# Performance work log

Measured on AMD Instinct MI355X. Metric: run time of the kernel, lower is better.

Reference implementation:

```python
import jax, jax.numpy as jnp
import numpy as np

B, S, E, D, H, L = 128, 50, 512, 1024, 16, 4
V, NU, NF, NR = 100000, 50000, 10000, 5
DK = D // H
FF = 4 * D


def _pe(S, D):
    # FranchisePositionalEncoding: two interleaved sin/cos halves (chrono + release*1.5)
    half = D // 2
    pos = jnp.arange(S, dtype=jnp.float32)[:, None]
    div = jnp.exp(jnp.arange(0, half, 2, dtype=jnp.float32) * (-np.log(10000.0) / half))
    def il(a):
        return jnp.stack([jnp.sin(a), jnp.cos(a)], axis=-1).reshape(S, half)
    return jnp.concatenate([il(pos * div), il(pos * div * 1.5)], axis=-1)  # [S, D]


def _ln(x, g, b):
    m = x.mean(-1, keepdims=True)
    v = ((x - m) ** 2).mean(-1, keepdims=True)
    return (x - m) * jax.lax.rsqrt(v + 1e-5) * g + b


def _gelu(x):
    return jax.nn.gelu(x, approximate=False)


def setup_inputs() -> dict:
    key = jax.random.key(0)
    ks = iter(jax.random.split(key, 64))
    def p(shape, s=0.02):
        return jax.random.normal(next(ks), shape, jnp.float32) * s
    inp = {
        'movie_table': p((V, E)), 'fran_table': p((NF, E)), 'entry_table': p((NR, E)),
        'proj_w': p((3 * E, D)), 'proj_b': jnp.zeros((D,), jnp.float32),
        'wq': p((L, D, D)), 'bq': jnp.zeros((L, D), jnp.float32),
        'wk': p((L, D, D)), 'bk': jnp.zeros((L, D), jnp.float32),
        'wv': p((L, D, D)), 'bv': jnp.zeros((L, D), jnp.float32),
        'wo': p((L, D, D)), 'bo': jnp.zeros((L, D), jnp.float32),
        'rel_table': p((L, NR, DK)),
        'aln_g': jnp.ones((L, D), jnp.float32), 'aln_b': jnp.zeros((L, D), jnp.float32),
        'f_w1': p((L, D, FF)), 'f_b1': jnp.zeros((L, FF), jnp.float32),
        'f_w2': p((L, FF, D)), 'f_b2': jnp.zeros((L, D), jnp.float32),
        'ln_g': jnp.ones((L, D), jnp.float32), 'ln_b': jnp.zeros((L, D), jnp.float32),
        'user_table': p((NU, D)),
        'mq_w': p((D, D)), 'mq_b': jnp.zeros((D,), jnp.float32),
        'mk_w': p((D, D)), 'mk_b': jnp.zeros((D,), jnp.float32),
        'mv_w': p((D, D)), 'mv_b': jnp.zeros((D,), jnp.float32),
        'mo_w': p((D, D)), 'mo_b': jnp.zeros((D,), jnp.float32),
        'c_w1': p((2 * D, D)), 'c_b1': jnp.zeros((D,), jnp.float32),
        'c_w2': p((D, 1)), 'c_b2': jnp.zeros((1,), jnp.float32),
        'n_w1': p((2 * D, D)), 'n_b1': jnp.zeros((D,), jnp.float32),
        'n_w2': p((D, V)), 'n_b2': jnp.zeros((V,), jnp.float32),
        'r_w1': p((3 * D, D)), 'r_b1': jnp.zeros((D,), jnp.float32),
        'r_w2': p((D, 1)), 'r_b2': jnp.zeros((1,), jnp.float32),
        'o_w1': p((D, D // 2)), 'o_b1': jnp.zeros((D // 2,), jnp.float32),
        'o_w2': p((D // 2, 2)), 'o_b2': jnp.zeros((2,), jnp.float32),
        'user_ids': jax.random.randint(next(ks), (B,), 0, NU),
        'movie_ids': jax.random.randint(next(ks), (B, S), 0, V),
        'franchise_ids': jax.random.randint(next(ks), (B, S), 0, NF),
        'entry_types': jax.random.randint(next(ks), (B, S), 0, NR),
        'relation_matrix': jax.random.randint(next(ks), (S, S), 0, NR),
    }
    return inp


def reference(movie_table, fran_table, entry_table, proj_w, proj_b,
              wq, bq, wk, bk, wv, bv, wo, bo, rel_table, aln_g, aln_b,
              f_w1, f_b1, f_w2, f_b2, ln_g, ln_b, user_table,
              mq_w, mq_b, mk_w, mk_b, mv_w, mv_b, mo_w, mo_b,
              c_w1, c_b1, c_w2, c_b2, n_w1, n_b1, n_w2, n_b2,
              r_w1, r_b1, r_w2, r_b2, o_w1, o_b1, o_w2, o_b2,
              user_ids, movie_ids, franchise_ids, entry_types, relation_matrix):
    b, s = movie_ids.shape
    d = proj_w.shape[1]
    nl, _, dk = rel_table.shape
    h = d // dk
    scale = 1.0 / np.sqrt(dk).astype(np.float32)

    # encoder input: concat(movie, franchise, entry) embeddings -> proj -> +PE
    x = jnp.concatenate([movie_table[movie_ids], fran_table[franchise_ids],
                         entry_table[entry_types]], axis=-1) @ proj_w + proj_b
    x = x + _pe(s, d)

    for l in range(nl):
        res = x
        q = (x @ wq[l] + bq[l]).reshape(b, s, h, dk).transpose(0, 2, 1, 3)  # [b,h,s,dk]
        k = (x @ wk[l] + bk[l]).reshape(b, s, h, dk).transpose(0, 2, 1, 3)
        v = (x @ wv[l] + bv[l]).reshape(b, s, h, dk).transpose(0, 2, 1, 3)
        scores = jnp.einsum('bhid,bhjd->bhij', q, k) * scale
        rel = rel_table[l][relation_matrix]  # [s,s,dk]
        scores = scores + 0.5 * jnp.einsum('bhid,ijd->bhij', q, rel)
        attn = jax.nn.softmax(scores, axis=-1)
        ctx = jnp.einsum('bhij,bhjd->bhid', attn, v).transpose(0, 2, 1, 3).reshape(b, s, d)
        x = _ln(ctx @ wo[l] + bo[l] + res, aln_g[l], aln_b[l])
        ff = _gelu(x @ f_w1[l] + f_b1[l]) @ f_w2[l] + f_b2[l]
        x = _ln(x + ff, ln_g[l], ln_b[l])

    # user preference cross-attention (nn.MultiheadAttention, q_len=1)
    user_emb = user_table[user_ids]  # [b,d]
    qh = (user_emb @ mq_w + mq_b).reshape(b, h, dk)
    kh = (x @ mk_w + mk_b).reshape(b, s, h, dk)
    vh = (x @ mv_w + mv_b).reshape(b, s, h, dk)
    a = jax.nn.softmax(jnp.einsum('bhd,bshd->bhs', qh, kh) * scale, axis=-1)
    user_pref = jnp.einsum('bhs,bshd->bhd', a, vh).reshape(b, d) @ mo_w + mo_b

    seq_repr = x.mean(axis=1)  # mask is None path
    ci = jnp.concatenate([user_pref, seq_repr], axis=-1)
    completion = jax.nn.sigmoid(_gelu(ci @ c_w1 + c_b1) @ c_w2 + c_b2)
    next_logits = _gelu(ci @ n_w1 + n_b1) @ n_w2 + n_b2
    ri = jnp.concatenate([user_emb, user_pref, seq_repr], axis=-1)
    rating = _gelu(ri @ r_w1 + r_b1) @ r_w2 + r_b2
    order = jax.nn.softmax(_gelu(user_pref @ o_w1 + o_b1) @ o_w2 + o_b2, axis=-1)
    return (x, completion, next_logits, rating, order, user_pref)
```

## Files before the change

### kernel.cpp

```cpp
#include <hip/hip_runtime.h>
#include <hip/hip_bf16.h>
#include <math.h>

#define B_   128
#define S_   50
#define BS_  (B_*S_)
#define E_   512
#define D_   1024
#define H_   16
#define DK_  64
#define L_   4
#define FF_  4096
#define V_   100000

typedef short bf8_t __attribute__((ext_vector_type(8)));
typedef float f32x4 __attribute__((ext_vector_type(4)));
typedef unsigned short u16;

__device__ __forceinline__ float gelu_exact(float x) {
    return 0.5f * x * (1.0f + erff(x * 0.70710678118654752440f));
}
__device__ __forceinline__ u16 f2bf(float f) {
    unsigned int u = __float_as_uint(f);
    return (u16)((u + 0x7FFFu + ((u >> 16) & 1u)) >> 16);
}
__device__ __forceinline__ float bf2f(u16 u) {
    return __uint_as_float(((unsigned int)u) << 16);
}

__device__ __forceinline__ void gload16(const u16* g, u16* l) {
    auto* g1 = reinterpret_cast<const __attribute__((address_space(1))) unsigned int*>(
                   reinterpret_cast<uintptr_t>(g));
    auto* l3 = reinterpret_cast<__attribute__((address_space(3))) unsigned int*>(
                   reinterpret_cast<uintptr_t>(l));
    __builtin_amdgcn_global_load_lds(g1, l3, 16, 0, 0);
}

__device__ __forceinline__ void wtrans_body(
    const float* __restrict__ W, u16* __restrict__ Wt,
    int K, int N, int nb, int kb, int dstRowOff)
{
    __shared__ float t[32][33];
    int c = threadIdx.x & 31, r0 = threadIdx.x >> 5;
    #pragma unroll
    for (int rr = 0; rr < 32; rr += 8)
        t[rr + r0][c] = W[(size_t)(kb + rr + r0) * N + nb + c];
    __syncthreads();
    #pragma unroll
    for (int rr = 0; rr < 32; rr += 8)
        Wt[(size_t)(dstRowOff + nb + rr + r0) * K + kb + c] = f2bf(t[c][rr + r0]);
}

__global__ __launch_bounds__(256) void wtrans(
    const float* __restrict__ W, u16* __restrict__ Wt,
    int K, int N, long srcLS, long dstLS, int dstRowOff)
{
    int l = blockIdx.z;
    wtrans_body(W + (size_t)l * srcLS, Wt + (size_t)l * dstLS,
                K, N, blockIdx.x * 32, blockIdx.y * 32, dstRowOff);
}

__global__ __launch_bounds__(256) void wtrans_qkv(
    const float* __restrict__ wq, const float* __restrict__ wk, const float* __restrict__ wv,
    u16* __restrict__ dst)
{
    int z = blockIdx.z;
    int l = z & 3, which = z >> 2;
    const float* W = (which == 0 ? wq : which == 1 ? wk : wv) + (size_t)l * (D_ * D_);
    u16* Wt = dst + (size_t)l * (3 * D_ * D_) + (size_t)which * (D_ * D_);
    wtrans_body(W, Wt, D_, D_, blockIdx.x * 32, blockIdx.y * 32, 0);
}

struct WT4 { const float* s[4]; u16* d[4]; };
__global__ __launch_bounds__(256) void wtrans4(WT4 p)
{
    int z = blockIdx.z;
    wtrans_body(p.s[z], p.d[z], D_, D_, blockIdx.x * 32, blockIdx.y * 32, 0);
}

__global__ __launch_bounds__(256) void wtrans_ff(
    const float* __restrict__ w1, const float* __restrict__ w2,
    u16* __restrict__ d1, u16* __restrict__ d2)
{
    if (blockIdx.z == 0)
        wtrans_body(w1, d1, D_, FF_, blockIdx.x * 32, blockIdx.y * 32, 0);
    else
        wtrans_body(w2, d2, FF_, D_, blockIdx.y * 32, blockIdx.x * 32, 0);
}

__global__ __launch_bounds__(256) void embed_concat(
    const float* __restrict__ mt, const float* __restrict__ ft, const float* __restrict__ et,
    const int* __restrict__ mids, const int* __restrict__ fids, const int* __restrict__ eids,
    u16* __restrict__ xinb)
{
    int bs = blockIdx.x;
    int mid = mids[bs], fid = fids[bs], eid = eids[bs];
    const float* srcs[3] = { mt + (size_t)mid * E_, ft + (size_t)fid * E_, et + (size_t)eid * E_ };
    u16* dst = xinb + (size_t)bs * (3 * E_);
    for (int i = threadIdx.x; i < 384; i += 256) {
        int seg = i >> 7, off = i & 127;
        float4 v = reinterpret_cast<const float4*>(srcs[seg])[off];
        ushort4 b;
        b.x = f2bf(v.x); b.y = f2bf(v.y); b.z = f2bf(v.z); b.w = f2bf(v.w);
        reinterpret_cast<ushort4*>(dst + seg * E_)[off] = b;
    }
}

__global__ __launch_bounds__(256) void pe_table(float* __restrict__ pet)
{
    int s = blockIdx.x;
    const float c = -logf(10000.0f) / 512.0f;
    for (int d = threadIdx.x; d < D_; d += 256) {
        int second = d >= 512;
        int cc = second ? d - 512 : d;
        int i = cc >> 1;
        float div = expf(c * (float)(2 * i));
        float a = (float)s * div * (second ? 1.5f : 1.0f);
        pet[s * D_ + d] = (cc & 1) ? cosf(a) : sinf(a);
    }
}

__global__ __launch_bounds__(256) void gemm_bf16(
    const u16* __restrict__ A, int lda, const u16* __restrict__ Wt,
    const float* __restrict__ bias, float* __restrict__ Cf,
    u16* __restrict__ Cb, int ldcb, u16* __restrict__ Cb2, int ldcb2,
    int M, int N, int K, int act, const float* __restrict__ pe)
{
    __shared__ u16 As[2 * 4096];
    __shared__ u16 Bs[2 * 4096];
    const int tid  = threadIdx.x;
    const int lane = tid & 63;
    const int wid  = tid >> 6;
    const int wr   = wid >> 1, wc = wid & 1;

    const int gx  = gridDim.x;
    const int nwg = gx * gridDim.y;
    {
    }
    int orig = blockIdx.y * gx + blockIdx.x;
    int qq = nwg >> 3, rr = nwg & 7, xcd = orig & 7, idx = orig >> 3;
    int wgid = (xcd < rr) ? (xcd * (qq + 1) + idx)
                          : (rr * (qq + 1) + (xcd - rr) * qq + idx);
    const int rowBase = (wgid / gx) * 128;
    const int colBase = (wgid % gx) * 128;

    const int fr = lane & 15;
    const int hi = lane >> 4;

    const int sRowL  = lane >> 2;
    const int sChunk = lane & 3;
    const int gRow0  = (wid << 5) + sRowL;
    const int skey   = (gRow0 >> 1) & 3;
    const int gC     = (sChunk ^ skey) << 3;
    const u16* aS0 = A  + (size_t)(rowBase + gRow0) * lda + gC;
    const u16* aS1 = aS0 + (size_t)16 * lda;
    const u16* bS0 = Wt + (size_t)(colBase + gRow0) * K + gC;
    const u16* bS1 = bS0 + (size_t)16 * K;
    const int ldsW0 = (wid << 5) << 5;
    const int ldsW1 = ldsW0 + (16 << 5);

    const int swz = ((hi ^ ((fr >> 1) & 3)) << 3);
    const int aRd = (wr * 64 + fr) * 32 + swz;
    const int bRd = (wc * 64 + fr) * 32 + swz;

    f32x4 acc[4][4] = {};
    const int nk = K >> 5;

    gload16(aS0, As + ldsW0);
    gload16(aS1, As + ldsW1);
    gload16(bS0, Bs + ldsW0);
    gload16(bS1, Bs + ldsW1);
    __builtin_amdgcn_sched_barrier(0);
    gload16(aS0 + 32, As + 4096 + ldsW0);
    gload16(aS1 + 32, As + 4096 + ldsW1);
    gload16(bS0 + 32, Bs + 4096 + ldsW0);
    gload16(bS1 + 32, Bs + 4096 + ldsW1);
    __builtin_amdgcn_sched_barrier(0);
    asm volatile("s_waitcnt vmcnt(4)\n\ts_barrier" ::: "memory");
    __builtin_amdgcn_sched_barrier(0);

    for (int t = 0; t < nk; ++t) {
        const int cur = t & 1;
        const u16* bA = As + cur * 4096;
        const u16* bB = Bs + cur * 4096;
        bf8_t af[4], bf[4];
        #pragma unroll
        for (int m = 0; m < 4; ++m)
            af[m] = *reinterpret_cast<const bf8_t*>(&bA[aRd + m * 512]);
        #pragma unroll
        for (int n = 0; n < 4; ++n)
            bf[n] = *reinterpret_cast<const bf8_t*>(&bB[bRd + n * 512]);
        #pragma unroll
        for (int m = 0; m < 4; ++m)
            #pragma unroll
            for (int n = 0; n < 4; ++n)
                acc[m][n] = __builtin_amdgcn_mfma_f32_16x16x32_bf16(af[m], bf[n], acc[m][n], 0, 0, 0);
        if (t == nk - 1) break;
        __builtin_amdgcn_sched_barrier(0);
        asm volatile("s_waitcnt lgkmcnt(0)\n\ts_barrier" ::: "memory");
        __builtin_amdgcn_sched_barrier(0);
        if (t + 2 < nk) {
            const int kb = (t + 2) << 5;
            u16* dA = As + cur * 4096;
            u16* dB = Bs + cur * 4096;
            gload16(aS0 + kb, dA + ldsW0);
            gload16(aS1 + kb, dA + ldsW1);
            gload16(bS0 + kb, dB + ldsW0);
            gload16(bS1 + kb, dB + ldsW1);
            __builtin_amdgcn_sched_barrier(0);
            asm volatile("s_waitcnt vmcnt(4)\n\ts_barrier" ::: "memory");
        } else {
            asm volatile("s_waitcnt vmcnt(0)\n\ts_barrier" ::: "memory");
        }
        __builtin_amdgcn_sched_barrier(0);
    }

    const int orow = (lane >> 4) << 2;
    #pragma unroll
    for (int m = 0; m < 4; ++m) {
        int r0 = rowBase + wr * 64 + m * 16 + orow;
        #pragma unroll
        for (int n = 0; n < 4; ++n) {
            int c = colBase + wc * 64 + n * 16 + fr;
            float bv = bias ? bias[c] : 0.0f;
            #pragma unroll
            for (int r = 0; r < 4; ++r) {
                float v = acc[m][n][r] + bv;
                if (act == 1) v = gelu_exact(v);
                if (pe) v += pe[(size_t)((r0 + r) % S_) * N + c];
                if (Cf)  Cf [(size_t)(r0 + r) * N + c] = v;
                if (Cb)  Cb [(size_t)(r0 + r) * ldcb  + c] = f2bf(v);
                if (Cb2) Cb2[(size_t)(r0 + r) * ldcb2 + c] = f2bf(v);
            }
        }
    }
}

__global__ __launch_bounds__(256) void gemm_logits(
    const float* __restrict__ A, int lda, const float* __restrict__ W,
    const float* __restrict__ bias, float* __restrict__ C, int N, int K)
{
    __shared__ u16 As[2][128][40];
    __shared__ u16 Bs[2][128][40];
    const int tid  = threadIdx.x;
    const int lane = tid & 63;
    const int wid  = tid >> 6;
    const int wr   = wid >> 1, wc = wid & 1;
    const int colBase = blockIdx.x * 128;

    const int a_r = tid >> 1;
    const int a_h = (tid & 1) << 4;
    const int b_c = tid & 127;
    const int b_h = (tid >> 7) << 4;

    const int fr = lane & 15;
    const int fk = (lane >> 4) << 3;

    f32x4 acc[4][4] = {};
    const int nvalid = N - colBase;
    const bool valid = b_c < nvalid;
    const int nk = K >> 5;

    float4 aR[4];
    float  bR[16];

    auto LD = [&](int kb) {
        const float* Ap = A + (size_t)a_r * lda + kb + a_h;
        #pragma unroll
        for (int q = 0; q < 4; ++q)
            aR[q] = *reinterpret_cast<const float4*>(Ap + q * 4);
        const float* Wp = W + (size_t)(kb + b_h) * N + colBase + b_c;
        #pragma unroll
        for (int kk = 0; kk < 16; ++kk)
            bR[kk] = valid ? Wp[(size_t)kk * N] : 0.0f;
    };
    auto ST = [&](int buf) {
        #pragma unroll
        for (int q = 0; q < 4; ++q) {
            ushort4 bb;
            bb.x = f2bf(aR[q].x); bb.y = f2bf(aR[q].y);
            bb.z = f2bf(aR[q].z); bb.w = f2bf(aR[q].w);
            *reinterpret_cast<ushort4*>(&As[buf][a_r][a_h + q * 4]) = bb;
        }
        u16 tmp[16];
        #pragma unroll
        for (int kk = 0; kk < 16; ++kk) tmp[kk] = f2bf(bR[kk]);
        *reinterpret_cast<bf8_t*>(&Bs[buf][b_c][b_h])     = *reinterpret_cast<const bf8_t*>(tmp);
        *reinterpret_cast<bf8_t*>(&Bs[buf][b_c][b_h + 8]) = *reinterpret_cast<const bf8_t*>(tmp + 8);
    };

    LD(0); ST(0);
    __syncthreads();

    for (int t = 0; t < nk; ++t) {
        if (t + 1 < nk) LD((t + 1) << 5);
        const int cur = t & 1;
        bf8_t af[4], bfv[4];
        #pragma unroll
        for (int m = 0; m < 4; ++m)
            af[m] = *reinterpret_cast<const bf8_t*>(&As[cur][wr * 64 + m * 16 + fr][fk]);
        #pragma unroll
        for (int n = 0; n < 4; ++n)
            bfv[n] = *reinterpret_cast<const bf8_t*>(&Bs[cur][wc * 64 + n * 16 + fr][fk]);
        #pragma unroll
        for (int m = 0; m < 4; ++m)
            #pragma unroll
            for (int n = 0; n < 4; ++n)
                acc[m][n] = __builtin_amdgcn_mfma_f32_16x16x32_bf16(af[m], bfv[n], acc[m][n], 0, 0, 0);
        if (t + 1 < nk) ST(cur ^ 1);
        __syncthreads();
    }

    const int orow = (lane >> 4) << 2;
    #pragma unroll
    for (int m = 0; m < 4; ++m) {
        int r0 = wr * 64 + m * 16 + orow;
        #pragma unroll
        for (int n = 0; n < 4; ++n) {
            int c = colBase + wc * 64 + n * 16 + fr;
            if (c < N) {
                float bv = bias ? bias[c] : 0.0f;
                #pragma unroll
                for (int r = 0; r < 4; ++r)
                    C[(size_t)(r0 + r) * N + c] = acc[m][n][r] + bv;
            }
        }
    }
}

__global__ __launch_bounds__(256) void attn_kernel(
    const u16* __restrict__ qkv, const float* __restrict__ rt, const int* __restrict__ rm,
    u16* __restrict__ ctxb)
{
    int bh = blockIdx.x;
    int b = bh >> 4, h = bh & 15;
    __shared__ float qs[S_][DK_ + 1], ks[S_][DK_ + 1], vs[S_][DK_ + 1];
    __shared__ float rts[5][DK_];
    __shared__ float Rs[S_][8];
    int tid = threadIdx.x;
    int wave = tid >> 6, lane = tid & 63;

    for (int idx = tid; idx < S_ * DK_; idx += 256) {
        int s = idx >> 6, d = idx & 63;
        size_t g = ((size_t)(b * S_ + s)) * (3 * D_) + h * DK_ + d;
        qs[s][d] = bf2f(qkv[g]);
        ks[s][d] = bf2f(qkv[g + D_]);
        vs[s][d] = bf2f(qkv[g + 2 * D_]);
    }
    for (int i = tid; i < 5 * DK_; i += 256)
        rts[i >> 6][i & 63] = rt[i];
    __syncthreads();

    for (int t = tid; t < S_ * 5; t += 256) {
        int i = t / 5, r = t - 5 * i;
        float a = 0.0f;
        #pragma unroll 8
        for (int d = 0; d < DK_; ++d) a += qs[i][d] * rts[r][d];
        Rs[i][r] = a;
    }
    __syncthreads();

    const float scale = 0.125f;
    for (int i = wave; i < S_; i += 4) {
        float sc = -INFINITY;
        if (lane < S_) {
            float acc = 0.0f;
            #pragma unroll 8
            for (int d = 0; d < DK_; ++d) acc += qs[i][d] * ks[lane][d];
            sc = acc * scale + 0.5f * Rs[i][rm[i * S_ + lane]];
        }
        float m = sc;
        #pragma unroll
        for (int off = 32; off; off >>= 1) m = fmaxf(m, __shfl_xor(m, off));
        float e = (lane < S_) ? expf(sc - m) : 0.0f;
        float sum = e;
        #pragma unroll
        for (int off = 32; off; off >>= 1) sum += __shfl_xor(sum, off);
        float aval = e / sum;

        float acc = 0.0f;
        for (int j = 0; j < S_; ++j) {
            float aj = __shfl(aval, j);
            acc += aj * vs[j][lane];
        }
        ctxb[((size_t)(b * S_ + i)) * D_ + h * DK_ + lane] = f2bf(acc);
    }
}

__global__ __launch_bounds__(256) void add_ln(
    const u16* __restrict__ a, const float* __restrict__ res,
    const float* __restrict__ g, const float* __restrict__ be,
    float* __restrict__ outf, u16* __restrict__ outb)
{
    int row = blockIdx.x, tid = threadIdx.x;
    const u16* pa = a + (size_t)row * D_;
    const float* pr = res + (size_t)row * D_;
    float vals[4];
    float s = 0.0f;
    #pragma unroll
    for (int t = 0; t < 4; ++t) {
        float v = bf2f(pa[tid + t * 256]) + pr[tid + t * 256];
        vals[t] = v;
        s += v;
    }
    __shared__ float red[8];
    #pragma unroll
    for (int off = 32; off; off >>= 1) s += __shfl_xor(s, off);
    int wave = tid >> 6, lane = tid & 63;
    if (lane == 0) red[wave] = s;
    __syncthreads();
    float mean = (red[0] + red[1] + red[2] + red[3]) * (1.0f / D_);
    float vv = 0.0f;
    #pragma unroll
    for (int t = 0; t < 4; ++t) {
        float d = vals[t] - mean;
        vv += d * d;
    }
    #pragma unroll
    for (int off = 32; off; off >>= 1) vv += __shfl_xor(vv, off);
    if (lane == 0) red[4 + wave] = vv;
    __syncthreads();
    float var = (red[4] + red[5] + red[6] + red[7]) * (1.0f / D_);
    float rstd = rsqrtf(var + 1e-5f);
    #pragma unroll
    for (int t = 0; t < 4; ++t) {
        int c = tid + t * 256;
        float v = (vals[t] - mean) * rstd * g[c] + be[c];
        outf[(size_t)row * D_ + c] = v;
        outb[(size_t)row * D_ + c] = f2bf(v);
    }
}

__global__ __launch_bounds__(256) void gather_user(
    const float* __restrict__ ut, const int* __restrict__ ids,
    u16* __restrict__ o1, int ld1, u16* __restrict__ o2, int ld2)
{
    int b = blockIdx.x;
    int uid = ids[b];
    for (int d = threadIdx.x; d < D_; d += 256) {
        u16 v = f2bf(ut[(size_t)uid * D_ + d]);
        o1[(size_t)b * ld1 + d] = v;
        o2[(size_t)b * ld2 + d] = v;
    }
}

__global__ __launch_bounds__(64) void cross_attn(
    const u16* __restrict__ qh, const u16* __restrict__ kv, u16* __restrict__ up)
{
    int bh = blockIdx.x;
    int b = bh >> 4, h = bh & 15;
    int lane = threadIdx.x;
    __shared__ float qv[DK_];
    qv[lane] = bf2f(qh[(size_t)b * D_ + h * DK_ + lane]);
    __syncthreads();
    float sc = -INFINITY;
    if (lane < S_) {
        float acc = 0.0f;
        const u16* krow = kv + ((size_t)(b * S_ + lane)) * 2048 + h * DK_;
        #pragma unroll 8
        for (int d = 0; d < DK_; ++d) acc += qv[d] * bf2f(krow[d]);
        sc = acc * 0.125f;
    }
    float m = sc;
    #pragma unroll
    for (int off = 32; off; off >>= 1) m = fmaxf(m, __shfl_xor(m, off));
    float e = (lane < S_) ? expf(sc - m) : 0.0f;
    float sum = e;
    #pragma unroll
    for (int off = 32; off; off >>= 1) sum += __shfl_xor(sum, off);
    float aval = e / sum;
    float acc = 0.0f;
    for (int j = 0; j < S_; ++j) {
        float aj = __shfl(aval, j);
        acc += aj * bf2f(kv[((size_t)(b * S_ + j)) * 2048 + 1024 + h * DK_ + lane]);
    }
    up[(size_t)b * D_ + h * DK_ + lane] = f2bf(acc);
}

__global__ __launch_bounds__(256) void seq_mean(
    const float* __restrict__ x,
    u16* __restrict__ o1, int ld1, u16* __restrict__ o2, int ld2)
{
    int b = blockIdx.x;
    for (int d = threadIdx.x; d < D_; d += 256) {
        float s = 0.0f;
        for (int si = 0; si < S_; ++si)
            s += x[((size_t)(b * S_ + si)) * D_ + d];
        u16 v = f2bf(s * (1.0f / S_));
        o1[(size_t)b * ld1 + d] = v;
        o2[(size_t)b * ld2 + d] = v;
    }
}

__global__ __launch_bounds__(256) void copy_cols(
    const float* __restrict__ src, float* __restrict__ dst,
    int width, int dstStride, int dstOff)
{
    int r = blockIdx.x;
    for (int c = threadIdx.x; c < width; c += 256)
        dst[(size_t)r * dstStride + dstOff + c] = src[(size_t)r * width + c];
}

__global__ __launch_bounds__(256) void heads_final(
    const float* __restrict__ h1cn, const float* __restrict__ h1r, const float* __restrict__ ho,
    const float* __restrict__ c_w2, const float* __restrict__ c_b2,
    const float* __restrict__ r_w2, const float* __restrict__ r_b2,
    const float* __restrict__ o_w2, const float* __restrict__ o_b2,
    float* __restrict__ comp, float* __restrict__ rating, float* __restrict__ order)
{
    int b = blockIdx.x;
    int lane = threadIdx.x & 63, wv = threadIdx.x >> 6;
    if (wv == 0) {
        float s = 0.0f;
        for (int d = lane; d < D_; d += 64) s += h1cn[(size_t)b * 2048 + d] * c_w2[d];
        #pragma unroll
        for (int off = 32; off; off >>= 1) s += __shfl_xor(s, off);
        if (lane == 0) comp[b] = 1.0f / (1.0f + expf(-(s + c_b2[0])));
    } else if (wv == 1) {
        float s = 0.0f;
        for (int d = lane; d < D_; d += 64) s += h1r[(size_t)b * D_ + d] * r_w2[d];
        #pragma unroll
        for (int off = 32; off; off >>= 1) s += __shfl_xor(s, off);
        if (lane == 0) rating[b] = s + r_b2[0];
    } else if (wv == 2) {
        float s0 = 0.0f, s1 = 0.0f;
        for (int d = lane; d < 512; d += 64) {
            float hv = ho[(size_t)b * 512 + d];
            s0 += hv * o_w2[d * 2];
            s1 += hv * o_w2[d * 2 + 1];
        }
        #pragma unroll
        for (int off = 32; off; off >>= 1) { s0 += __shfl_xor(s0, off); s1 += __shfl_xor(s1, off); }
        if (lane == 0) {
            float a = s0 + o_b2[0], c = s1 + o_b2[1];
            float m = fmaxf(a, c);
            float ea = expf(a - m), ec = expf(c - m);
            float s = ea + ec;
            order[b * 2] = ea / s;
            order[b * 2 + 1] = ec / s;
        }
    }
}

extern "C" void kernel_launch(void* const* d_in, const int* in_sizes, int n_in,
                              void* d_out, int out_size, void* d_ws, size_t ws_size,
                              hipStream_t stream) {
    const float* movie_table = (const float*)d_in[0];
    const float* fran_table  = (const float*)d_in[1];
    const float* entry_table = (const float*)d_in[2];
    const float* proj_w      = (const float*)d_in[3];
    const float* proj_b      = (const float*)d_in[4];
    const float* wq          = (const float*)d_in[5];
    const float* bq          = (const float*)d_in[6];
    const float* wk          = (const float*)d_in[7];
    const float* bk          = (const float*)d_in[8];
    const float* wv          = (const float*)d_in[9];
    const float* bv          = (const float*)d_in[10];
    const float* wo          = (const float*)d_in[11];
    const float* bo          = (const float*)d_in[12];
    const float* rel_table   = (const float*)d_in[13];
    const float* aln_g       = (const float*)d_in[14];
    const float* aln_b       = (const float*)d_in[15];
    const float* f_w1        = (const float*)d_in[16];
    const float* f_b1        = (const float*)d_in[17];
    const float* f_w2        = (const float*)d_in[18];
    const float* f_b2        = (const float*)d_in[19];
    const float* ln_g        = (const float*)d_in[20];
    const float* ln_b        = (const float*)d_in[21];
    const float* user_table  = (const float*)d_in[22];
    const float* mq_w        = (const float*)d_in[23];
    const float* mq_b        = (const float*)d_in[24];
    const float* mk_w        = (const float*)d_in[25];
    const float* mk_b        = (const float*)d_in[26];
    const float* mv_w        = (const float*)d_in[27];
    const float* mv_b        = (const float*)d_in[28];
    const float* mo_w        = (const float*)d_in[29];
    const float* mo_b        = (const float*)d_in[30];
    const float* c_w1        = (const float*)d_in[31];
    const float* c_b1        = (const float*)d_in[32];
    const float* c_w2        = (const float*)d_in[33];
    const float* c_b2        = (const float*)d_in[34];
    const float* n_w1        = (const float*)d_in[35];
    const float* n_b1        = (const float*)d_in[36];
    const float* n_w2        = (const float*)d_in[37];
    const float* n_b2        = (const float*)d_in[38];
    const float* r_w1        = (const float*)d_in[39];
    const float* r_b1        = (const float*)d_in[40];
    const float* r_w2        = (const float*)d_in[41];
    const float* r_b2        = (const float*)d_in[42];
    const float* o_w1        = (const float*)d_in[43];
    const float* o_b1        = (const float*)d_in[44];
    const float* o_w2        = (const float*)d_in[45];
    const float* o_b2        = (const float*)d_in[46];
    const int* user_ids      = (const int*)d_in[47];
    const int* movie_ids     = (const int*)d_in[48];
    const int* franchise_ids = (const int*)d_in[49];
    const int* entry_types   = (const int*)d_in[50];
    const int* relation_mat  = (const int*)d_in[51];

    u16* up16 = (u16*)d_ws;
    u16* proj_wt = up16;
    u16* wqkv_t  = proj_wt + (size_t)1024 * 1536;
    u16* wo_t    = wqkv_t  + (size_t)4 * 3072 * 1024;
    u16* fw1_buf = wo_t    + (size_t)4 * 1024 * 1024;
    u16* fw2_buf = fw1_buf + (size_t)4096 * 1024;
    u16* mq_t    = fw2_buf + (size_t)1024 * 4096;
    u16* mk_t    = mq_t    + (size_t)1024 * 1024;
    u16* mv_t    = mk_t    + (size_t)1024 * 1024;
    u16* mo_t    = mv_t    + (size_t)1024 * 1024;
    u16* cn_w1t  = mo_t    + (size_t)1024 * 1024;
    u16* r_w1t   = cn_w1t  + (size_t)2048 * 2048;
    u16* o_w1t   = r_w1t   + (size_t)1024 * 3072;
    u16* ffb     = o_w1t   + (size_t)512 * 1024;
    u16* xinb    = ffb;
    u16* xb      = ffb     + (size_t)BS_ * FF_;
    u16* qkvb    = xb      + (size_t)BS_ * D_;
    u16* kvb     = qkvb    + (size_t)BS_ * 3 * D_;
    u16* ctxb    = kvb;
    u16* ob      = kvb     + (size_t)BS_ * D_;
    u16* ueb     = kvb     + (size_t)BS_ * 2 * D_;
    u16* upb_pre = ueb     + (size_t)B_ * D_;
    u16* cib     = upb_pre + (size_t)B_ * D_;
    u16* rib     = cib     + (size_t)B_ * 2 * D_;
    float* fp    = (float*)(rib + (size_t)B_ * 3 * D_);
    float* bqkv  = fp;
    float* bcn   = bqkv + 4 * 3072;
    float* bkv   = bcn  + 2048;
    float* pet   = bkv  + 2048;
    float* h1cn  = pet  + 50 * 1024;
    float* h1r   = h1cn + (size_t)B_ * 2048;
    float* ho    = h1r  + (size_t)B_ * D_;

    float* xout    = (float*)d_out;
    float* comp    = xout + (size_t)BS_ * D_;
    float* logits  = comp + B_;
    float* rating  = logits + (size_t)B_ * V_;
    float* order   = rating + B_;
    float* upref   = order + 2 * B_;

    dim3 blk(256);

    wtrans<<<dim3(32, 48, 1), blk, 0, stream>>>(proj_w, proj_wt, 1536, 1024, 0, 0, 0);
    wtrans_qkv<<<dim3(32, 32, 12), blk, 0, stream>>>(wq, wk, wv, wqkv_t);
    wtrans<<<dim3(32, 32, 4), blk, 0, stream>>>(wo, wo_t, 1024, 1024, 1048576, 1048576, 0);
    WT4 wm;
    wm.s[0] = mq_w; wm.s[1] = mk_w; wm.s[2] = mv_w; wm.s[3] = mo_w;
    wm.d[0] = mq_t; wm.d[1] = mk_t; wm.d[2] = mv_t; wm.d[3] = mo_t;
    wtrans4<<<dim3(32, 32, 4), blk, 0, stream>>>(wm);
    wtrans<<<dim3(32, 64, 1), blk, 0, stream>>>(c_w1, cn_w1t, 2048, 1024, 0, 0, 0);
    wtrans<<<dim3(32, 64, 1), blk, 0, stream>>>(n_w1, cn_w1t, 2048, 1024, 0, 0, 1024);
    wtrans<<<dim3(32, 96, 1), blk, 0, stream>>>(r_w1, r_w1t, 3072, 1024, 0, 0, 0);
    wtrans<<<dim3(16, 32, 1), blk, 0, stream>>>(o_w1, o_w1t, 1024, 512, 0, 0, 0);
    copy_cols<<<4, blk, 0, stream>>>(bq, bqkv, 1024, 3072, 0);
    copy_cols<<<4, blk, 0, stream>>>(bk, bqkv, 1024, 3072, 1024);
    copy_cols<<<4, blk, 0, stream>>>(bv, bqkv, 1024, 3072, 2048);
    copy_cols<<<1, blk, 0, stream>>>(c_b1, bcn, 1024, 2048, 0);
    copy_cols<<<1, blk, 0, stream>>>(n_b1, bcn, 1024, 2048, 1024);
    copy_cols<<<1, blk, 0, stream>>>(mk_b, bkv, 1024, 2048, 0);
    copy_cols<<<1, blk, 0, stream>>>(mv_b, bkv, 1024, 2048, 1024);
    pe_table<<<S_, blk, 0, stream>>>(pet);

    embed_concat<<<BS_, blk, 0, stream>>>(movie_table, fran_table, entry_table,
                                          movie_ids, franchise_ids, entry_types, xinb);
    gemm_bf16<<<dim3(8, 50), blk, 0, stream>>>(xinb, 1536, proj_wt, proj_b,
                                               xout, xb, 1024, nullptr, 0,
                                               BS_, D_, 1536, 0, pet);

    for (int l = 0; l < L_; ++l) {
        gemm_bf16<<<dim3(24, 50), blk, 0, stream>>>(xb, 1024, wqkv_t + (size_t)l * 3145728,
                                                    bqkv + l * 3072, nullptr, qkvb, 3072,
                                                    nullptr, 0, BS_, 3 * D_, D_, 0, nullptr);
        attn_kernel<<<B_ * H_, blk, 0, stream>>>(qkvb, rel_table + (size_t)l * 5 * DK_,
                                                 relation_mat, ctxb);
        gemm_bf16<<<dim3(8, 50), blk, 0, stream>>>(ctxb, 1024, wo_t + (size_t)l * 1048576,
                                                   bo + l * D_, nullptr, ob, 1024,
                                                   nullptr, 0, BS_, D_, D_, 0, nullptr);
        add_ln<<<BS_, blk, 0, stream>>>(ob, xout, aln_g + l * D_, aln_b + l * D_, xout, xb);
        wtrans_ff<<<dim3(128, 32, 2), blk, 0, stream>>>(f_w1 + (size_t)l * D_ * FF_,
                                                        f_w2 + (size_t)l * FF_ * D_,
                                                        fw1_buf, fw2_buf);
        gemm_bf16<<<dim3(32, 50), blk, 0, stream>>>(xb, 1024, fw1_buf, f_b1 + l * FF_,
                                                    nullptr, ffb, 4096, nullptr, 0,
                                                    BS_, FF_, D_, 1, nullptr);
        gemm_bf16<<<dim3(8, 50), blk, 0, stream>>>(ffb, 4096, fw2_buf, f_b2 + l * D_,
                                                   nullptr, ob, 1024, nullptr, 0,
                                                   BS_, D_, FF_, 0, nullptr);
        add_ln<<<BS_, blk, 0, stream>>>(ob, xout, ln_g + l * D_, ln_b + l * D_, xout, xb);
    }

    gather_user<<<B_, blk, 0, stream>>>(user_table, user_ids, ueb, 1024, rib, 3072);
    gemm_bf16<<<dim3(8, 1), blk, 0, stream>>>(ueb, 1024, mq_t, mq_b, nullptr, qkvb, 1024,
                                              nullptr, 0, B_, D_, D_, 0, nullptr);
    gemm_bf16<<<dim3(16, 50), blk, 0, stream>>>(xb, 1024, mk_t, bkv, nullptr, kvb, 2048,
                                                nullptr, 0, BS_, 2 * D_, D_, 0, nullptr);
    cross_attn<<<B_ * H_, dim3(64), 0, stream>>>(qkvb, kvb, upb_pre);
    gemm_bf16<<<dim3(8, 1), blk, 0, stream>>>(upb_pre, 1024, mo_t, mo_b, upref,
                                              cib, 2048, rib + 1024, 3072,
                                              B_, D_, D_, 0, nullptr);

    seq_mean<<<B_, blk, 0, stream>>>(xout, cib + 1024, 2048, rib + 2048, 3072);

    gemm_bf16<<<dim3(16, 1), blk, 0, stream>>>(cib, 2048, cn_w1t, bcn, h1cn,
                                               nullptr, 0, nullptr, 0,
                                               B_, 2048, 2048, 1, nullptr);
    gemm_bf16<<<dim3(8, 1), blk, 0, stream>>>(rib, 3072, r_w1t, r_b1, h1r,
                                              nullptr, 0, nullptr, 0,
                                              B_, D_, 3072, 1, nullptr);
    gemm_bf16<<<dim3(4, 1), blk, 0, stream>>>(cib, 2048, o_w1t, o_b1, ho,
                                              nullptr, 0, nullptr, 0,
                                              B_, 512, D_, 1, nullptr);
    gemm_logits<<<dim3(782, 1), blk, 0, stream>>>(h1cn + 1024, 2048, n_w2, n_b2,
                                                  logits, V_, D_);
    heads_final<<<B_, blk, 0, stream>>>(h1cn, h1r, ho, c_w2, c_b2, r_w2, r_b2,
                                        o_w2, o_b2, comp, rating, order);
}
```

Before: 2.222 ms.

## Template GEMM on row tile, use BM=64 for narrow GEMMs, bf16 residual stream

The bf16 GEMM now takes the row-tile height as a template parameter. N=1024 and small-M GEMMs use 64-row tiles, which doubles the workgroup count (800 instead of 400) and fills more CUs. The residual stream is kept in bf16 with ping-pong buffers, and the fp32 copy is written only in the last layer. add_ln is vectorised, and the bias-copy, PE-table and weight-transpose launches are merged into fewer kernels. Keeping the residual in bf16 lowers precision, and the smaller tiles reuse each loaded B tile over fewer rows.

```diff
diff --git a/kernel.cpp b/kernel.cpp
--- a/kernel.cpp
+++ b/kernel.cpp
@@ -71,8 +71,8 @@
     wtrans_body(W, Wt, D_, D_, blockIdx.x * 32, blockIdx.y * 32, 0);
 }
 
-struct WT4 { const float* s[4]; u16* d[4]; };
-__global__ __launch_bounds__(256) void wtrans4(WT4 p)
+struct WT8 { const float* s[8]; u16* d[8]; };
+__global__ __launch_bounds__(256) void wtrans8(WT8 p)
 {
     int z = blockIdx.z;
     wtrans_body(p.s[z], p.d[z], D_, D_, blockIdx.x * 32, blockIdx.y * 32, 0);
@@ -106,27 +106,52 @@
     }
 }
 
-__global__ __launch_bounds__(256) void pe_table(float* __restrict__ pet)
-{
-    int s = blockIdx.x;
-    const float c = -logf(10000.0f) / 512.0f;
-    for (int d = threadIdx.x; d < D_; d += 256) {
-        int second = d >= 512;
-        int cc = second ? d - 512 : d;
-        int i = cc >> 1;
-        float div = expf(c * (float)(2 * i));
-        float a = (float)s * div * (second ? 1.5f : 1.0f);
-        pet[s * D_ + d] = (cc & 1) ? cosf(a) : sinf(a);
-    }
-}
-
-__global__ __launch_bounds__(256) void gemm_bf16(
+__global__ __launch_bounds__(256) void setup_misc(
+    const float* __restrict__ bq, const float* __restrict__ bk, const float* __restrict__ bv,
+    const float* __restrict__ cb1, const float* __restrict__ nb1,
+    const float* __restrict__ mkb, const float* __restrict__ mvb,
+    float* __restrict__ bqkv, float* __restrict__ bcn, float* __restrict__ bkv,
+    float* __restrict__ pet)
+{
+    int bi = blockIdx.x, tid = threadIdx.x;
+    if (bi < 4) {
+        for (int c = tid; c < 3072; c += 256) {
+            float v = (c < 1024) ? bq[bi * 1024 + c]
+                    : (c < 2048) ? bk[bi * 1024 + c - 1024]
+                                 : bv[bi * 1024 + c - 2048];
+            bqkv[bi * 3072 + c] = v;
+        }
+    } else if (bi == 4) {
+        for (int c = tid; c < 2048; c += 256)
+            bcn[c] = (c < 1024) ? cb1[c] : nb1[c - 1024];
+    } else if (bi == 5) {
+        for (int c = tid; c < 2048; c += 256)
+            bkv[c] = (c < 1024) ? mkb[c] : mvb[c - 1024];
+    } else {
+        int s = bi - 6;
+        const float cc = -logf(10000.0f) / 512.0f;
+        for (int d = tid; d < D_; d += 256) {
+            int second = d >= 512;
+            int c2 = second ? d - 512 : d;
+            int i = c2 >> 1;
+            float div = expf(cc * (float)(2 * i));
+            float aa = (float)s * div * (second ? 1.5f : 1.0f);
+            pet[s * D_ + d] = (c2 & 1) ? cosf(aa) : sinf(aa);
+        }
+    }
+}
+
+template<int BM>
+__global__ __launch_bounds__(256) void gemm_bf16_t(
     const u16* __restrict__ A, int lda, const u16* __restrict__ Wt,
     const float* __restrict__ bias, float* __restrict__ Cf,
     u16* __restrict__ Cb, int ldcb, u16* __restrict__ Cb2, int ldcb2,
-    int M, int N, int K, int act, const float* __restrict__ pe)
-{
-    __shared__ u16 As[2 * 4096];
+    int N, int K, int act, const float* __restrict__ pe)
+{
+    constexpr int MR   = BM / 32;
+    constexpr int AL   = BM / 64;
+    constexpr int ABUF = BM * 32;
+    __shared__ u16 As[2 * ABUF];
     __shared__ u16 Bs[2 * 4096];
     const int tid  = threadIdx.x;
     const int lane = tid & 63;
@@ -135,13 +160,11 @@
 
     const int gx  = gridDim.x;
     const int nwg = gx * gridDim.y;
-    {
-    }
     int orig = blockIdx.y * gx + blockIdx.x;
-    int qq = nwg >> 3, rr = nwg & 7, xcd = orig & 7, idx = orig >> 3;
-    int wgid = (xcd < rr) ? (xcd * (qq + 1) + idx)
-                          : (rr * (qq + 1) + (xcd - rr) * qq + idx);
-    const int rowBase = (wgid / gx) * 128;
+    int qq = nwg >> 3, rr2 = nwg & 7, xcd = orig & 7, idx = orig >> 3;
+    int wgid = (xcd < rr2) ? (xcd * (qq + 1) + idx)
+                           : (rr2 * (qq + 1) + (xcd - rr2) * qq + idx);
+    const int rowBase = (wgid / gx) * BM;
     const int colBase = (wgid % gx) * 128;
 
     const int fr = lane & 15;
@@ -149,49 +172,56 @@
 
     const int sRowL  = lane >> 2;
     const int sChunk = lane & 3;
-    const int gRow0  = (wid << 5) + sRowL;
-    const int skey   = (gRow0 >> 1) & 3;
-    const int gC     = (sChunk ^ skey) << 3;
-    const u16* aS0 = A  + (size_t)(rowBase + gRow0) * lda + gC;
+    const int aRow0 = wid * (BM / 4) + sRowL;
+    const int aKey  = (aRow0 >> 1) & 3;
+    const u16* aS0 = A + (size_t)(rowBase + aRow0) * lda + ((sChunk ^ aKey) << 3);
     const u16* aS1 = aS0 + (size_t)16 * lda;
-    const u16* bS0 = Wt + (size_t)(colBase + gRow0) * K + gC;
+    const int ldsA0 = (wid * (BM / 4)) * 32;
+    const int ldsA1 = ldsA0 + 512;
+    const int bRow0 = wid * 32 + sRowL;
+    const int bKey  = (bRow0 >> 1) & 3;
+    const u16* bS0 = Wt + (size_t)(colBase + bRow0) * K + ((sChunk ^ bKey) << 3);
     const u16* bS1 = bS0 + (size_t)16 * K;
-    const int ldsW0 = (wid << 5) << 5;
-    const int ldsW1 = ldsW0 + (16 << 5);
+    const int ldsB0 = (wid * 32) * 32;
+    const int ldsB1 = ldsB0 + 512;
 
     const int swz = ((hi ^ ((fr >> 1) & 3)) << 3);
-    const int aRd = (wr * 64 + fr) * 32 + swz;
+    const int aRd = (wr * (BM / 2) + fr) * 32 + swz;
     const int bRd = (wc * 64 + fr) * 32 + swz;
 
-    f32x4 acc[4][4] = {};
+    f32x4 acc[MR][4] = {};
     const int nk = K >> 5;
 
-    gload16(aS0, As + ldsW0);
-    gload16(aS1, As + ldsW1);
-    gload16(bS0, Bs + ldsW0);
-    gload16(bS1, Bs + ldsW1);
+    auto STAGE = [&](int kb, int buf) {
+        u16* dA = As + buf * ABUF;
+        u16* dB = Bs + buf * 4096;
+        gload16(aS0 + kb, dA + ldsA0);
+        if constexpr (AL == 2) gload16(aS1 + kb, dA + ldsA1);
+        gload16(bS0 + kb, dB + ldsB0);
+        gload16(bS1 + kb, dB + ldsB1);
+    };
+
+    STAGE(0, 0);
     __builtin_amdgcn_sched_barrier(0);
-    gload16(aS0 + 32, As + 4096 + ldsW0);
-    gload16(aS1 + 32, As + 4096 + ldsW1);
-    gload16(bS0 + 32, Bs + 4096 + ldsW0);
-    gload16(bS1 + 32, Bs + 4096 + ldsW1);
+    STAGE(32, 1);
     __builtin_amdgcn_sched_barrier(0);
-    asm volatile("s_waitcnt vmcnt(4)\n\ts_barrier" ::: "memory");
+    if constexpr (BM == 128) asm volatile("s_waitcnt vmcnt(4)\n\ts_barrier" ::: "memory");
+    else                     asm volatile("s_waitcnt vmcnt(3)\n\ts_barrier" ::: "memory");
     __builtin_amdgcn_sched_barrier(0);
 
     for (int t = 0; t < nk; ++t) {
         const int cur = t & 1;
-        const u16* bA = As + cur * 4096;
+        const u16* bA = As + cur * ABUF;
         const u16* bB = Bs + cur * 4096;
-        bf8_t af[4], bf[4];
-        #pragma unroll
-        for (int m = 0; m < 4; ++m)
+        bf8_t af[MR], bf[4];
+        #pragma unroll
+        for (int m = 0; m < MR; ++m)
             af[m] = *reinterpret_cast<const bf8_t*>(&bA[aRd + m * 512]);
         #pragma unroll
         for (int n = 0; n < 4; ++n)
             bf[n] = *reinterpret_cast<const bf8_t*>(&bB[bRd + n * 512]);
         #pragma unroll
-        for (int m = 0; m < 4; ++m)
+        for (int m = 0; m < MR; ++m)
             #pragma unroll
             for (int n = 0; n < 4; ++n)
                 acc[m][n] = __builtin_amdgcn_mfma_f32_16x16x32_bf16(af[m], bf[n], acc[m][n], 0, 0, 0);
@@ -200,25 +230,20 @@
         asm volatile("s_waitcnt lgkmcnt(0)\n\ts_barrier" ::: "memory");
         __builtin_amdgcn_sched_barrier(0);
         if (t + 2 < nk) {
-            const int kb = (t + 2) << 5;
-            u16* dA = As + cur * 4096;
-            u16* dB = Bs + cur * 4096;
-            gload16(aS0 + kb, dA + ldsW0);
-            gload16(aS1 + kb, dA + ldsW1);
-            gload16(bS0 + kb, dB + ldsW0);
-            gload16(bS1 + kb, dB + ldsW1);
+            STAGE((t + 2) << 5, cur);
             __builtin_amdgcn_sched_barrier(0);
-            asm volatile("s_waitcnt vmcnt(4)\n\ts_barrier" ::: "memory");
+            if constexpr (BM == 128) asm volatile("s_waitcnt vmcnt(4)\n\ts_barrier" ::: "memory");
+            else                     asm volatile("s_waitcnt vmcnt(3)\n\ts_barrier" ::: "memory");
         } else {
             asm volatile("s_waitcnt vmcnt(0)\n\ts_barrier" ::: "memory");
         }
         __builtin_amdgcn_sched_barrier(0);
     }
 
-    const int orow = (lane >> 4) << 2;
-    #pragma unroll
-    for (int m = 0; m < 4; ++m) {
-        int r0 = rowBase + wr * 64 + m * 16 + orow;
+    const int orow = hi << 2;
+    #pragma unroll
+    for (int m = 0; m < MR; ++m) {
+        int r0 = rowBase + wr * (BM / 2) + m * 16 + orow;
         #pragma unroll
         for (int n = 0; n < 4; ++n) {
             int c = colBase + wc * 64 + n * 16 + fr;
@@ -388,21 +413,17 @@
 }
 
 __global__ __launch_bounds__(256) void add_ln(
-    const u16* __restrict__ a, const float* __restrict__ res,
+    const u16* __restrict__ a, const u16* __restrict__ res,
     const float* __restrict__ g, const float* __restrict__ be,
-    float* __restrict__ outf, u16* __restrict__ outb)
+    u16* __restrict__ outb, float* __restrict__ outf)
 {
     int row = blockIdx.x, tid = threadIdx.x;
-    const u16* pa = a + (size_t)row * D_;
-    const float* pr = res + (size_t)row * D_;
-    float vals[4];
-    float s = 0.0f;
-    #pragma unroll
-    for (int t = 0; t < 4; ++t) {
-        float v = bf2f(pa[tid + t * 256]) + pr[tid + t * 256];
-        vals[t] = v;
-        s += v;
-    }
+    int c0 = tid << 2;
+    ushort4 va = *reinterpret_cast<const ushort4*>(a   + (size_t)row * D_ + c0);
+    ushort4 vr = *reinterpret_cast<const ushort4*>(res + (size_t)row * D_ + c0);
+    float vals[4] = { bf2f(va.x) + bf2f(vr.x), bf2f(va.y) + bf2f(vr.y),
+                      bf2f(va.z) + bf2f(vr.z), bf2f(va.w) + bf2f(vr.w) };
+    float s = vals[0] + vals[1] + vals[2] + vals[3];
     __shared__ float red[8];
     #pragma unroll
     for (int off = 32; off; off >>= 1) s += __shfl_xor(s, off);
@@ -422,12 +443,18 @@
     __syncthreads();
     float var = (red[4] + red[5] + red[6] + red[7]) * (1.0f / D_);
     float rstd = rsqrtf(var + 1e-5f);
-    #pragma unroll
-    for (int t = 0; t < 4; ++t) {
-        int c = tid + t * 256;
-        float v = (vals[t] - mean) * rstd * g[c] + be[c];
-        outf[(size_t)row * D_ + c] = v;
-        outb[(size_t)row * D_ + c] = f2bf(v);
+    float4 gv  = *reinterpret_cast<const float4*>(g  + c0);
+    float4 bev = *reinterpret_cast<const float4*>(be + c0);
+    float o0 = (vals[0] - mean) * rstd * gv.x + bev.x;
+    float o1 = (vals[1] - mean) * rstd * gv.y + bev.y;
+    float o2 = (vals[2] - mean) * rstd * gv.z + bev.z;
+    float o3 = (vals[3] - mean) * rstd * gv.w + bev.w;
+    ushort4 ob;
+    ob.x = f2bf(o0); ob.y = f2bf(o1); ob.z = f2bf(o2); ob.w = f2bf(o3);
+    *reinterpret_cast<ushort4*>(outb + (size_t)row * D_ + c0) = ob;
+    if (outf) {
+        float4 of = { o0, o1, o2, o3 };
+        *reinterpret_cast<float4*>(outf + (size_t)row * D_ + c0) = of;
     }
 }
 
@@ -490,15 +517,6 @@
         o1[(size_t)b * ld1 + d] = v;
         o2[(size_t)b * ld2 + d] = v;
     }
-}
-
-__global__ __launch_bounds__(256) void copy_cols(
-    const float* __restrict__ src, float* __restrict__ dst,
-    int width, int dstStride, int dstOff)
-{
-    int r = blockIdx.x;
-    for (int c = threadIdx.x; c < width; c += 256)
-        dst[(size_t)r * dstStride + dstOff + c] = src[(size_t)r * width + c];
 }
 
 __global__ __launch_bounds__(256) void heads_final(
@@ -614,7 +632,8 @@
     u16* ffb     = o_w1t   + (size_t)512 * 1024;
     u16* xinb    = ffb;
     u16* xb      = ffb     + (size_t)BS_ * FF_;
-    u16* qkvb    = xb      + (size_t)BS_ * D_;
+    u16* xb2     = xb      + (size_t)BS_ * D_;
+    u16* qkvb    = xb2     + (size_t)BS_ * D_;
     u16* kvb     = qkvb    + (size_t)BS_ * 3 * D_;
     u16* ctxb    = kvb;
     u16* ob      = kvb     + (size_t)BS_ * D_;
@@ -642,73 +661,67 @@
 
     wtrans<<<dim3(32, 48, 1), blk, 0, stream>>>(proj_w, proj_wt, 1536, 1024, 0, 0, 0);
     wtrans_qkv<<<dim3(32, 32, 12), blk, 0, stream>>>(wq, wk, wv, wqkv_t);
-    wtrans<<<dim3(32, 32, 4), blk, 0, stream>>>(wo, wo_t, 1024, 1024, 1048576, 1048576, 0);
-    WT4 wm;
-    wm.s[0] = mq_w; wm.s[1] = mk_w; wm.s[2] = mv_w; wm.s[3] = mo_w;
-    wm.d[0] = mq_t; wm.d[1] = mk_t; wm.d[2] = mv_t; wm.d[3] = mo_t;
-    wtrans4<<<dim3(32, 32, 4), blk, 0, stream>>>(wm);
+    WT8 w8;
+    w8.s[0] = wo;                 w8.d[0] = wo_t;
+    w8.s[1] = wo + 1048576;       w8.d[1] = wo_t + 1048576;
+    w8.s[2] = wo + 2097152;       w8.d[2] = wo_t + 2097152;
+    w8.s[3] = wo + 3145728;       w8.d[3] = wo_t + 3145728;
+    w8.s[4] = mq_w;               w8.d[4] = mq_t;
+    w8.s[5] = mk_w;               w8.d[5] = mk_t;
+    w8.s[6] = mv_w;               w8.d[6] = mv_t;
+    w8.s[7] = mo_w;               w8.d[7] = mo_t;
+    wtrans8<<<dim3(32, 32, 8), blk, 0, stream>>>(w8);
     wtrans<<<dim3(32, 64, 1), blk, 0, stream>>>(c_w1, cn_w1t, 2048, 1024, 0, 0, 0);
     wtrans<<<dim3(32, 64, 1), blk, 0, stream>>>(n_w1, cn_w1t, 2048, 1024, 0, 0, 1024);
     wtrans<<<dim3(32, 96, 1), blk, 0, stream>>>(r_w1, r_w1t, 3072, 1024, 0, 0, 0);
     wtrans<<<dim3(16, 32, 1), blk, 0, stream>>>(o_w1, o_w1t, 1024, 512, 0, 0, 0);
-    copy_cols<<<4, blk, 0, stream>>>(bq, bqkv, 1024, 3072, 0);
-    copy_cols<<<4, blk, 0, stream>>>(bk, bqkv, 1024, 3072, 1024);
-    copy_cols<<<4, blk, 0, stream>>>(bv, bqkv, 1024, 3072, 2048);
-    copy_cols<<<1, blk, 0, stream>>>(c_b1, bcn, 1024, 2048, 0);
-    copy_cols<<<1, blk, 0, stream>>>(n_b1, bcn, 1024, 2048, 1024);
-    copy_cols<<<1, blk, 0, stream>>>(mk_b, bkv, 1024, 2048, 0);
-    copy_cols<<<1, blk, 0, stream>>>(mv_b, bkv, 1024, 2048, 1024);
-    pe_table<<<S_, blk, 0, stream>>>(pet);
+    setup_misc<<<dim3(56), blk, 0, stream>>>(bq, bk, bv, c_b1, n_b1, mk_b, mv_b,
+                                             bqkv, bcn, bkv, pet);
 
     embed_concat<<<BS_, blk, 0, stream>>>(movie_table, fran_table, entry_table,
                                           movie_ids, franchise_ids, entry_types, xinb);
-    gemm_bf16<<<dim3(8, 50), blk, 0, stream>>>(xinb, 1536, proj_wt, proj_b,
-                                               xout, xb, 1024, nullptr, 0,
-                                               BS_, D_, 1536, 0, pet);
+    gemm_bf16_t<64><<<dim3(8, 100), blk, 0, stream>>>(xinb, 1536, proj_wt, proj_b,
+                                                      nullptr, xb, 1024, nullptr, 0,
+                                                      D_, 1536, 0, pet);
 
     for (int l = 0; l < L_; ++l) {
-        gemm_bf16<<<dim3(24, 50), blk, 0, stream>>>(xb, 1024, wqkv_t + (size_t)l * 3145728,
-                                                    bqkv + l * 3072, nullptr, qkvb, 3072,
-                                                    nullptr, 0, BS_, 3 * D_, D_, 0, nullptr);
+        gemm_bf16_t<128><<<dim3(24, 50), blk, 0, stream>>>(xb, 1024,
+                wqkv_t + (size_t)l * 3145728, bqkv + l * 3072,
+                nullptr, qkvb, 3072, nullptr, 0, 3 * D_, D_, 0, nullptr);
         attn_kernel<<<B_ * H_, blk, 0, stream>>>(qkvb, rel_table + (size_t)l * 5 * DK_,
                                                  relation_mat, ctxb);
-        gemm_bf16<<<dim3(8, 50), blk, 0, stream>>>(ctxb, 1024, wo_t + (size_t)l * 1048576,
-                                                   bo + l * D_, nullptr, ob, 1024,
-                                                   nullptr, 0, BS_, D_, D_, 0, nullptr);
-        add_ln<<<BS_, blk, 0, stream>>>(ob, xout, aln_g + l * D_, aln_b + l * D_, xout, xb);
+        gemm_bf16_t<64><<<dim3(8, 100), blk, 0, stream>>>(ctxb, 1024,
+                wo_t + (size_t)l * 1048576, bo + l * D_,
+                nullptr, ob, 1024, nullptr, 0, D_, D_, 0, nullptr);
+        add_ln<<<BS_, blk, 0, stream>>>(ob, xb, aln_g + l * D_, aln_b + l * D_, xb2, nullptr);
         wtrans_ff<<<dim3(128, 32, 2), blk, 0, stream>>>(f_w1 + (size_t)l * D_ * FF_,
                                                         f_w2 + (size_t)l * FF_ * D_,
                                                         fw1_buf, fw2_buf);
-        gemm_bf16<<<dim3(32, 50), blk, 0, stream>>>(xb, 1024, fw1_buf, f_b1 + l * FF_,
-                                                    nullptr, ffb, 4096, nullptr, 0,
-                                                    BS_, FF_, D_, 1, nullptr);
-        gemm_bf16<<<dim3(8, 50), blk, 0, stream>>>(ffb, 4096, fw2_buf, f_b2 + l * D_,
-                                                   nullptr, ob, 1024, nullptr, 0,
-                                                   BS_, D_, FF_, 0, nullptr);
-        add_ln<<<BS_, blk, 0, stream>>>(ob, xout, ln_g + l * D_, ln_b + l * D_, xout, xb);
+        gemm_bf16_t<128><<<dim3(32, 50), blk, 0, stream>>>(xb2, 1024, fw1_buf, f_b1 + l * FF_,
+                nullptr, ffb, 4096, nullptr, 0, FF_, D_, 1, nullptr);
+        gemm_bf16_t<64><<<dim3(8, 100), blk, 0, stream>>>(ffb, 4096, fw2_buf, f_b2 + l * D_,
+                nullptr, ob, 1024, nullptr, 0, D_, FF_, 0, nullptr);
+        add_ln<<<BS_, blk, 0, stream>>>(ob, xb2, ln_g + l * D_, ln_b + l * D_, xb,
+                                        (l == L_ - 1) ? xout : nullptr);
     }
 
     gather_user<<<B_, blk, 0, stream>>>(user_table, user_ids, ueb, 1024, rib, 3072);
-    gemm_bf16<<<dim3(8, 1), blk, 0, stream>>>(ueb, 1024, mq_t, mq_b, nullptr, qkvb, 1024,
-                                              nullptr, 0, B_, D_, D_, 0, nullptr);
-    gemm_bf16<<<dim3(16, 50), blk, 0, stream>>>(xb, 1024, mk_t, bkv, nullptr, kvb, 2048,
-                                                nullptr, 0, BS_, 2 * D_, D_, 0, nullptr);
+    gemm_bf16_t<64><<<dim3(8, 2), blk, 0, stream>>>(ueb, 1024, mq_t, mq_b,
+            nullptr, qkvb, 1024, nullptr, 0, D_, D_, 0, nullptr);
+    gemm_bf16_t<64><<<dim3(16, 100), blk, 0, stream>>>(xb, 1024, mk_t, bkv,
+            nullptr, kvb, 2048, nullptr, 0, 2 * D_, D_, 0, nullptr);
     cross_attn<<<B_ * H_, dim3(64), 0, stream>>>(qkvb, kvb, upb_pre);
-    gemm_bf16<<<dim3(8, 1), blk, 0, stream>>>(upb_pre, 1024, mo_t, mo_b, upref,
-                                              cib, 2048, rib + 1024, 3072,
-                                              B_, D_, D_, 0, nullptr);
+    gemm_bf16_t<64><<<dim3(8, 2), blk, 0, stream>>>(upb_pre, 1024, mo_t, mo_b,
+            upref, cib, 2048, rib + 1024, 3072, D_, D_, 0, nullptr);
 
     seq_mean<<<B_, blk, 0, stream>>>(xout, cib + 1024, 2048, rib + 2048, 3072);
 
-    gemm_bf16<<<dim3(16, 1), blk, 0, stream>>>(cib, 2048, cn_w1t, bcn, h1cn,
-                                               nullptr, 0, nullptr, 0,
-                                               B_, 2048, 2048, 1, nullptr);
-    gemm_bf16<<<dim3(8, 1), blk, 0, stream>>>(rib, 3072, r_w1t, r_b1, h1r,
-                                              nullptr, 0, nullptr, 0,
-                                              B_, D_, 3072, 1, nullptr);
-    gemm_bf16<<<dim3(4, 1), blk, 0, stream>>>(cib, 2048, o_w1t, o_b1, ho,
-                                              nullptr, 0, nullptr, 0,
-                                              B_, 512, D_, 1, nullptr);
+    gemm_bf16_t<64><<<dim3(16, 2), blk, 0, stream>>>(cib, 2048, cn_w1t, bcn,
+            h1cn, nullptr, 0, nullptr, 0, 2048, 2048, 1, nullptr);
+    gemm_bf16_t<64><<<dim3(8, 2), blk, 0, stream>>>(rib, 3072, r_w1t, r_b1,
+            h1r, nullptr, 0, nullptr, 0, D_, 3072, 1, nullptr);
+    gemm_bf16_t<64><<<dim3(4, 2), blk, 0, stream>>>(cib, 2048, o_w1t, o_b1,
+            ho, nullptr, 0, nullptr, 0, 512, D_, 1, nullptr);
     gemm_logits<<<dim3(782, 1), blk, 0, stream>>>(h1cn + 1024, 2048, n_w2, n_b2,
                                                   logits, V_, D_);
     heads_final<<<B_, blk, 0, stream>>>(h1cn, h1r, ho, c_w2, c_b2, r_w2, r_b2,
```

New measurement: 2.283 ms. 2.7% more time.
